# Performance work log

Measured on AMD Instinct MI355X. Metric: run time of the kernel, lower is better.

## Reference

```python
import jax, jax.numpy as jnp
import numpy as np

NUM_EMBEDDINGS = 4096
EMBEDDING_DIM = 128
COMMITMENT_COST = 0.25


def setup_inputs() -> dict:
    key = jax.random.key(0)
    k_x, k_w = jax.random.split(key)
    inputs = jax.random.normal(k_x, (32, 128, 32, 32), dtype=jnp.float32)
    # xavier_uniform for Embedding weight [K, D]: bound = sqrt(6/(K+D))
    bound = float(np.sqrt(6.0 / (NUM_EMBEDDINGS + EMBEDDING_DIM)))
    weight = jax.random.uniform(k_w, (NUM_EMBEDDINGS, EMBEDDING_DIM),
                                dtype=jnp.float32, minval=-bound, maxval=bound)
    return {"inputs": inputs, "weight": weight}


def reference(inputs, weight):
    K, D = weight.shape
    # channels-first 4D input with C == embedding_dim -> NHWC
    x = jnp.transpose(inputs, (0, 2, 3, 1))  # [B, H, W, D]
    input_shape = x.shape
    flat = x.reshape(-1, D)                  # [N, D]

    x_sq = jnp.sum(flat * flat, axis=1, keepdims=True)          # [N, 1]
    w_sq = jnp.sum(weight * weight, axis=1)                     # [K]
    two_xy = 2.0 * jnp.matmul(flat, weight.T)                   # [N, K]
    distances = x_sq - two_xy + w_sq[None, :] + 1e-8

    encoding_indices = jnp.argmin(distances, axis=1)            # [N] int

    quantized = weight[encoding_indices].reshape(input_shape)   # [B, H, W, D]

    q_latent_loss = jnp.mean((quantized - x) ** 2)
    e_latent_loss = jnp.mean((jax.lax.stop_gradient(quantized) - x) ** 2)
    loss = q_latent_loss + COMMITMENT_COST * e_latent_loss
    loss = jnp.where(jnp.isnan(loss) | jnp.isinf(loss), jnp.float32(0.1), loss)

    quantized_st = x + jax.lax.stop_gradient(quantized - x)

    counts = jnp.zeros((K,), dtype=jnp.float32).at[encoding_indices].add(1.0)
    avg_probs = counts / encoding_indices.shape[0]
    perplexity = jnp.exp(-jnp.sum(avg_probs * jnp.log(avg_probs + 1e-10)))

    encodings = jax.nn.one_hot(encoding_indices, K, dtype=jnp.float32)  # [N, K]

    # input was channels-first -> restore NCHW
    quantized_st = jnp.transpose(quantized_st, (0, 3, 1, 2))
    return quantized_st, loss, perplexity, encodings, encoding_indices
```

## Files before the change

### kernel.cpp

```cpp
#include <hip/hip_runtime.h>
#include <stdint.h>
#include <math.h>

#define K_CODES 4096
#define DIM 128
#define N_FLAT 32768
#define HW 1024

#define OFF_Q    0
#define OFF_LOSS 4194304
#define OFF_PERP 4194305
#define OFF_ENC  4194306
#define OFF_IDX  138412034

#define WS_PACKED 0
#define WS_COUNTS 262144
#define WS_WSQ    278528
#define WS_XSQ    294912
#define WS_PART   425984
#define WS_XHL    430080
#define WS_WHL    (WS_XHL + 16777216)

typedef _Float16 f16x8 __attribute__((ext_vector_type(8)));
typedef float    f32x4 __attribute__((ext_vector_type(4)));


__global__ __launch_bounds__(256) void wsq_kernel(const float* __restrict__ w,
                                                  float* __restrict__ wsq,
                                                  float* __restrict__ counts) {
    int wave = threadIdx.x >> 6, lane = threadIdx.x & 63;
    int k = blockIdx.x * 4 + wave;
    float a = w[k * DIM + lane];
    float b = w[k * DIM + lane + 64];
    float s = a * a + b * b;
    #pragma unroll
    for (int o = 32; o > 0; o >>= 1) s += __shfl_down(s, o, 64);
    if (lane == 0) { wsq[k] = s; counts[k] = 0.f; }
}

__global__ __launch_bounds__(256) void wplanes_kernel(const float* __restrict__ w,
                                                      _Float16* __restrict__ whl) {
    int T = blockIdx.x * 256 + threadIdx.x;
    int k = T >> 2, seg = T & 3;
    const float* wp = w + (size_t)k * DIM + seg * 32;
    _Float16* row = whl + (size_t)k * 256;
    #pragma unroll
    for (int q = 0; q < 4; ++q) {
        float4 a = *(const float4*)(wp + q * 8);
        float4 b = *(const float4*)(wp + q * 8 + 4);
        float vv[8] = {a.x, a.y, a.z, a.w, b.x, b.y, b.z, b.w};
        f16x8 hv, lv;
        #pragma unroll
        for (int j = 0; j < 8; ++j) {
            float v = 1024.0f * vv[j];
            _Float16 h = (_Float16)v;
            _Float16 l = (_Float16)(v - (float)h);
            hv[j] = h; lv[j] = l;
        }
        *(f16x8*)(row + seg * 32 + q * 8) = hv;
        *(f16x8*)(row + 128 + seg * 32 + q * 8) = lv;
    }
}

__global__ __launch_bounds__(256) void xprep_kernel(const float* __restrict__ x,
                                                    _Float16* __restrict__ xhl,
                                                    float* __restrict__ xsq,
                                                    unsigned long long* __restrict__ packed) {
    __shared__ float xt[128 * 65];
    const int t = threadIdx.x;
    const int n0 = blockIdx.x * 64;
    const int b = n0 >> 10, hw0 = n0 & 1023;
    const float* xg = x + (size_t)b * (DIM * HW) + hw0;
    #pragma unroll
    for (int i = 0; i < 16; ++i) {
        int idx = i * 256 + t;
        int c = idx >> 5, n2 = (idx & 31) << 1;
        float2 v = *(const float2*)(xg + c * HW + n2);
        xt[c * 65 + n2] = v.x;
        xt[c * 65 + n2 + 1] = v.y;
    }
    __syncthreads();
    if (t < 64) {
        packed[n0 + t] = ~0ull;
        float s = 0.f;
        #pragma unroll
        for (int c = 0; c < DIM; ++c) {
            float v = xt[c * 65 + t];
            s = fmaf(v, v, s);
        }
        xsq[n0 + t] = s;
    }
    const int n = t >> 2, seg = t & 3;
    _Float16* row = xhl + (size_t)(n0 + n) * 256;
    #pragma unroll
    for (int q = 0; q < 4; ++q) {
        f16x8 hv, lv;
        #pragma unroll
        for (int j = 0; j < 8; ++j) {
            float v = 32.0f * xt[(seg * 32 + q * 8 + j) * 65 + n];
            _Float16 h = (_Float16)v;
            _Float16 l = (_Float16)(v - (float)h);
            hv[j] = h; lv[j] = l;
        }
        *(f16x8*)(row + seg * 32 + q * 8) = hv;
        *(f16x8*)(row + 128 + seg * 32 + q * 8) = lv;
    }
}

__global__ __launch_bounds__(512) void dist_argmin(
    const _Float16* __restrict__ xhl, const _Float16* __restrict__ whl,
    const float* __restrict__ wsq, const float* __restrict__ xsq,
    unsigned long long* __restrict__ packed, float* __restrict__ enc)
{
    __shared__ __align__(16) char xlds[2][16384];
    __shared__ __align__(16) char wlds[2][16384];
    __shared__ float xsq_s[128];
    __shared__ unsigned long long red[128];

    const int tid  = threadIdx.x;
    const int lane = tid & 63, wave = tid >> 6;
    const int lq   = lane & 15, quad = lane >> 4;
    const int wn0  = (wave >> 2) * 64;
    const int wk0q = (wave & 3) * 32;
    const int n0   = blockIdx.x * 128;
    const int kbase = blockIdx.y * 512;

    const int r0 = wave * 16 + (lane >> 3);
    const int lc = (((lane & 7) ^ (lane >> 3)) << 4);
    const int lcAdj = lc + ((lc >> 6) * 192);
    const char* xB = (const char*)xhl;
    const char* wB = (const char*)whl;
    const size_t xrow0 = (size_t)(n0 + r0) * 512;

    const int swz  = (lq & 7) << 4;
    const int hoff = (quad << 4) ^ swz;
    const int loff = (64 | (quad << 4)) ^ swz;

    float* ebase = enc + (size_t)n0 * K_CODES + kbase;
    if (tid < 128) {
        float2 z2; z2.x = 0.f; z2.y = 0.f;
        *(float2*)(ebase + (size_t)tid * K_CODES) = z2;
        xsq_s[tid] = xsq[n0 + tid];
        red[tid] = ~0ull;
    }

#define GLOAD16(gp, lp) __builtin_amdgcn_global_load_lds(                      \
        (const __attribute__((address_space(1))) void*)(gp),                   \
        (__attribute__((address_space(3))) void*)(lp), 16, 0, 0)

    {
        const size_t wrow0 = (size_t)(kbase + r0) * 512;
        #pragma unroll
        for (int i = 0; i < 2; ++i) {
            GLOAD16(xB + xrow0 + (size_t)i * 4096 + lcAdj,
                    xlds[0] + wave * 2048 + i * 1024);
            GLOAD16(wB + wrow0 + (size_t)i * 4096 + lcAdj,
                    wlds[0] + wave * 2048 + i * 1024);
        }
    }

    f32x4 acc[4][2];
    float wk[2];

    for (int s = 0; s < 16; ++s) {
        const int p  = s & 1;
        const int ks = s >> 2, c0 = s & 3;
        const int k0 = kbase + ks * 128;
        if (c0 == 0) {
            wk[0] = wsq[k0 + wk0q + lq];
            wk[1] = wsq[k0 + wk0q + 16 + lq];
            #pragma unroll
            for (int i = 0; i < 4; ++i)
                #pragma unroll
                for (int j = 0; j < 2; ++j)
                    acc[i][j] = (f32x4){0.f, 0.f, 0.f, 0.f};
        }
        __syncthreads();

        f16x8 ah[4], al[4], bh[2], bl[2];
        const char* xb = xlds[p];
        const char* wb = wlds[p];
        #pragma unroll
        for (int i = 0; i < 4; ++i) {
            int xr = (wn0 + 16 * i + lq) * 128;
            ah[i] = *(const f16x8*)(xb + xr + hoff);
            al[i] = *(const f16x8*)(xb + xr + loff);
        }
        #pragma unroll
        for (int ki = 0; ki < 2; ++ki) {
            int wr = (wk0q + 16 * ki + lq) * 128;
            bh[ki] = *(const f16x8*)(wb + wr + hoff);
            bl[ki] = *(const f16x8*)(wb + wr + loff);
        }

        if (s < 15) {
            const int s1 = s + 1, ks1 = s1 >> 2, c01 = s1 & 3;
            const int offX = c01 * 64 + lcAdj;
            const size_t wrow0 = (size_t)(kbase + ks1 * 128 + r0) * 512;
            char* xd = xlds[p ^ 1] + wave * 2048;
            char* wd = wlds[p ^ 1] + wave * 2048;
            #pragma unroll
            for (int i = 0; i < 2; ++i) {
                GLOAD16(xB + xrow0 + (size_t)i * 4096 + offX, xd + i * 1024);
                GLOAD16(wB + wrow0 + (size_t)i * 4096 + offX, wd + i * 1024);
            }
        }

        {
            float4 z4; z4.x = z4.y = z4.z = z4.w = 0.f;
            #pragma unroll
            for (int j = 0; j < 2; ++j) {
                int idx = s * 1024 + j * 512 + tid;
                int r = idx >> 7, c4 = idx & 127;
                *(float4*)(ebase + (size_t)r * K_CODES + 2 + c4 * 4) = z4;
            }
        }

        #pragma unroll
        for (int ki = 0; ki < 2; ++ki)
            #pragma unroll
            for (int ni = 0; ni < 4; ++ni) {
                acc[ni][ki] = __builtin_amdgcn_mfma_f32_16x16x32_f16(
                    ah[ni], bh[ki], acc[ni][ki], 0, 0, 0);
                acc[ni][ki] = __builtin_amdgcn_mfma_f32_16x16x32_f16(
                    ah[ni], bl[ki], acc[ni][ki], 0, 0, 0);
                acc[ni][ki] = __builtin_amdgcn_mfma_f32_16x16x32_f16(
                    al[ni], bh[ki], acc[ni][ki], 0, 0, 0);
            }

        if (c0 == 3) {
            #pragma unroll
            for (int ni = 0; ni < 4; ++ni) {
                #pragma unroll
                for (int rg = 0; rg < 4; ++rg) {
                    int rowl = wn0 + ni * 16 + quad * 4 + rg;
                    float xr = xsq_s[rowl];
                    float best = 3.4e38f; int bk = 0;
                    #pragma unroll
                    for (int ki = 0; ki < 2; ++ki) {
                        int kl = wk0q + ki * 16 + lq;
                        float t = xr - acc[ni][ki][rg] * 6.103515625e-05f;
                        t += wk[ki];
                        t += 1e-8f;
                        if (t < best) { best = t; bk = k0 + kl; }
                    }
                    unsigned u = __float_as_uint(best);
                    u = (u & 0x80000000u) ? ~u : (u | 0x80000000u);
                    unsigned long long pck =
                        ((unsigned long long)u << 32) | (unsigned)bk;
                    #pragma unroll
                    for (int m = 1; m < 16; m <<= 1) {
                        unsigned long long o = __shfl_xor(pck, m, 64);
                        if (o < pck) pck = o;
                    }
                    if (lq == 0) atomicMin(&red[rowl], pck);
                }
            }
        }
    }
#undef GLOAD16

    __syncthreads();
    if (tid < 128) atomicMin(&packed[n0 + tid], red[tid]);
}

__global__ __launch_bounds__(256) void combine(
    const unsigned long long* __restrict__ packed,
    float* __restrict__ idxf, float* __restrict__ enc,
    float* __restrict__ counts)
{
    int n = blockIdx.x * 256 + threadIdx.x;
    unsigned k = (unsigned)(packed[n] & 0xFFFFFFFFu);
    idxf[n] = (float)k;
    enc[(size_t)n * K_CODES + k] = 1.0f;
    atomicAdd(&counts[k], 1.0f);
}

__global__ __launch_bounds__(256) void quantize_loss(
    const float* __restrict__ x, const float* __restrict__ w,
    const float* __restrict__ idxf, float* __restrict__ outq,
    float* __restrict__ part)
{
    const int base4 = (blockIdx.x * 256 + threadIdx.x) * 4;
    float s = 0.f;
    #pragma unroll
    for (int i = 0; i < 4; ++i) {
        int e  = base4 + i * 1048576;
        int hw = e & 1023;
        int c  = (e >> 10) & 127;
        int b  = e >> 17;
        int n  = (b << 10) | hw;
        float4 xv = *(const float4*)(x + e);
        float4 kf = *(const float4*)(idxf + n);
        float q0 = w[(int)kf.x * DIM + c];
        float q1 = w[(int)kf.y * DIM + c];
        float q2 = w[(int)kf.z * DIM + c];
        float q3 = w[(int)kf.w * DIM + c];
        float4 df; df.x = q0 - xv.x; df.y = q1 - xv.y;
                   df.z = q2 - xv.z; df.w = q3 - xv.w;
        float4 o;  o.x = xv.x + df.x; o.y = xv.y + df.y;
                   o.z = xv.z + df.z; o.w = xv.w + df.w;
        *(float4*)(outq + e) = o;
        s = fmaf(df.x, df.x, s);
        s = fmaf(df.y, df.y, s);
        s = fmaf(df.z, df.z, s);
        s = fmaf(df.w, df.w, s);
    }
    #pragma unroll
    for (int o = 32; o > 0; o >>= 1) s += __shfl_down(s, o, 64);
    __shared__ float ls[4];
    if ((threadIdx.x & 63) == 0) ls[threadIdx.x >> 6] = s;
    __syncthreads();
    if (threadIdx.x == 0) part[blockIdx.x] = ls[0] + ls[1] + ls[2] + ls[3];
}

__global__ __launch_bounds__(256) void finalize(
    const float* __restrict__ counts, const float* __restrict__ part,
    float* __restrict__ out)
{
    __shared__ float sh[512];
    float h = 0.f;
    for (int k = threadIdx.x; k < K_CODES; k += 256) {
        float p = counts[k] * (1.0f / N_FLAT);
        h += p * logf(p + 1e-10f);
    }
    float s = 0.f;
    for (int i = threadIdx.x; i < 1024; i += 256) s += part[i];
    sh[threadIdx.x] = h;
    sh[256 + threadIdx.x] = s;
    __syncthreads();
    #pragma unroll
    for (int st = 128; st > 0; st >>= 1) {
        if (threadIdx.x < st) {
            sh[threadIdx.x] += sh[threadIdx.x + st];
            sh[256 + threadIdx.x] += sh[256 + threadIdx.x + st];
        }
        __syncthreads();
    }
    if (threadIdx.x == 0) {
        float perp = expf(-sh[0]);
        float loss = 1.25f * (sh[256] / 4194304.0f);
        if (isnan(loss) || isinf(loss)) loss = 0.1f;
        out[OFF_LOSS] = loss;
        out[OFF_PERP] = perp;
    }
}

extern "C" void kernel_launch(void* const* d_in, const int* in_sizes, int n_in,
                              void* d_out, int out_size, void* d_ws, size_t ws_size,
                              hipStream_t stream) {
    const float* x = (const float*)d_in[0];
    const float* w = (const float*)d_in[1];
    float* out = (float*)d_out;
    char* ws = (char*)d_ws;

    unsigned long long* packed = (unsigned long long*)(ws + WS_PACKED);
    float* counts = (float*)(ws + WS_COUNTS);
    float* wsq    = (float*)(ws + WS_WSQ);
    float* xsq    = (float*)(ws + WS_XSQ);
    float* part   = (float*)(ws + WS_PART);
    _Float16* xhl = (_Float16*)(ws + WS_XHL);
    _Float16* whl = (_Float16*)(ws + WS_WHL);

    wsq_kernel<<<K_CODES / 4, 256, 0, stream>>>(w, wsq, counts);
    wplanes_kernel<<<K_CODES * 4 / 256, 256, 0, stream>>>(w, whl);
    xprep_kernel<<<N_FLAT / 64, 256, 0, stream>>>(x, xhl, xsq, packed);

    dim3 g2(256, 8);
    dist_argmin<<<g2, 512, 0, stream>>>(xhl, whl, wsq, xsq, packed,
                                        out + OFF_ENC);

    combine<<<N_FLAT / 256, 256, 0, stream>>>(packed, out + OFF_IDX,
                                              out + OFF_ENC, counts);

    quantize_loss<<<1024, 256, 0, stream>>>(x, w, out + OFF_IDX,
                                            out + OFF_Q, part);

    finalize<<<1, 256, 0, stream>>>(counts, part, out);
}
```

Measured before the change: 766.1 us.

## Widen code-range per block and remap grid for XCD-aware locality

Each block now covers 1024 codes instead of 512, halving the grid to 1024 blocks and doubling the K-loop to 32 stages. The 1D block index is remapped so consecutive x-tiles land on the same XCD, which should improve L2 reuse of the x data. The A-fragment LDS loads are moved inside the MFMA loop to cut register pressure. The encoding zero-fill is re-indexed to cover the wider code range. The risk is fewer blocks for load balance and extra LDS reads being exposed instead of hidden.

```diff
diff --git a/kernel.cpp b/kernel.cpp
--- a/kernel.cpp
+++ b/kernel.cpp
@@ -122,8 +122,13 @@
     const int lq   = lane & 15, quad = lane >> 4;
     const int wn0  = (wave >> 2) * 64;
     const int wk0q = (wave & 3) * 32;
-    const int n0   = blockIdx.x * 128;
-    const int kbase = blockIdx.y * 512;
+
+    const int id  = blockIdx.x;
+    const int xcd = id & 7, q = id >> 3;
+    const int y   = q & 3;
+    const int t   = (q >> 2) * 8 + xcd;
+    const int n0    = t * 128;
+    const int kbase = y * 1024;
 
     const int r0 = wave * 16 + (lane >> 3);
     const int lc = (((lane & 7) ^ (lane >> 3)) << 4);
@@ -162,7 +167,7 @@
     f32x4 acc[4][2];
     float wk[2];
 
-    for (int s = 0; s < 16; ++s) {
+    for (int s = 0; s < 32; ++s) {
         const int p  = s & 1;
         const int ks = s >> 2, c0 = s & 3;
         const int k0 = kbase + ks * 128;
@@ -177,15 +182,10 @@
         }
         __syncthreads();
 
-        f16x8 ah[4], al[4], bh[2], bl[2];
         const char* xb = xlds[p];
         const char* wb = wlds[p];
-        #pragma unroll
-        for (int i = 0; i < 4; ++i) {
-            int xr = (wn0 + 16 * i + lq) * 128;
-            ah[i] = *(const f16x8*)(xb + xr + hoff);
-            al[i] = *(const f16x8*)(xb + xr + loff);
-        }
+
+        f16x8 bh[2], bl[2];
         #pragma unroll
         for (int ki = 0; ki < 2; ++ki) {
             int wr = (wk0q + 16 * ki + lq) * 128;
@@ -193,7 +193,7 @@
             bl[ki] = *(const f16x8*)(wb + wr + loff);
         }
 
-        if (s < 15) {
+        if (s < 31) {
             const int s1 = s + 1, ks1 = s1 >> 2, c01 = s1 & 3;
             const int offX = c01 * 64 + lcAdj;
             const size_t wrow0 = (size_t)(kbase + ks1 * 128 + r0) * 512;
@@ -211,22 +211,26 @@
             #pragma unroll
             for (int j = 0; j < 2; ++j) {
                 int idx = s * 1024 + j * 512 + tid;
-                int r = idx >> 7, c4 = idx & 127;
+                int r = idx >> 8, c4 = idx & 255;
                 *(float4*)(ebase + (size_t)r * K_CODES + 2 + c4 * 4) = z4;
             }
         }
 
         #pragma unroll
-        for (int ki = 0; ki < 2; ++ki)
-            #pragma unroll
-            for (int ni = 0; ni < 4; ++ni) {
+        for (int ni = 0; ni < 4; ++ni) {
+            int xr = (wn0 + 16 * ni + lq) * 128;
+            f16x8 ah = *(const f16x8*)(xb + xr + hoff);
+            f16x8 al = *(const f16x8*)(xb + xr + loff);
+            #pragma unroll
+            for (int ki = 0; ki < 2; ++ki) {
                 acc[ni][ki] = __builtin_amdgcn_mfma_f32_16x16x32_f16(
-                    ah[ni], bh[ki], acc[ni][ki], 0, 0, 0);
+                    ah, bh[ki], acc[ni][ki], 0, 0, 0);
                 acc[ni][ki] = __builtin_amdgcn_mfma_f32_16x16x32_f16(
-                    ah[ni], bl[ki], acc[ni][ki], 0, 0, 0);
+                    ah, bl[ki], acc[ni][ki], 0, 0, 0);
                 acc[ni][ki] = __builtin_amdgcn_mfma_f32_16x16x32_f16(
-                    al[ni], bh[ki], acc[ni][ki], 0, 0, 0);
+                    al, bh[ki], acc[ni][ki], 0, 0, 0);
             }
+        }
 
         if (c0 == 3) {
             #pragma unroll
@@ -239,10 +243,10 @@
                     #pragma unroll
                     for (int ki = 0; ki < 2; ++ki) {
                         int kl = wk0q + ki * 16 + lq;
-                        float t = xr - acc[ni][ki][rg] * 6.103515625e-05f;
-                        t += wk[ki];
-                        t += 1e-8f;
-                        if (t < best) { best = t; bk = k0 + kl; }
+                        float tt = xr - acc[ni][ki][rg] * 6.103515625e-05f;
+                        tt += wk[ki];
+                        tt += 1e-8f;
+                        if (tt < best) { best = tt; bk = k0 + kl; }
                     }
                     unsigned u = __float_as_uint(best);
                     u = (u & 0x80000000u) ? ~u : (u | 0x80000000u);
@@ -366,9 +370,8 @@
     wplanes_kernel<<<K_CODES * 4 / 256, 256, 0, stream>>>(w, whl);
     xprep_kernel<<<N_FLAT / 64, 256, 0, stream>>>(x, xhl, xsq, packed);
 
-    dim3 g2(256, 8);
-    dist_argmin<<<g2, 512, 0, stream>>>(xhl, whl, wsq, xsq, packed,
-                                        out + OFF_ENC);
+    dist_argmin<<<1024, 512, 0, stream>>>(xhl, whl, wsq, xsq, packed,
+                                          out + OFF_ENC);
 
     combine<<<N_FLAT / 256, 256, 0, stream>>>(packed, out + OFF_IDX,
                                               out + OFF_ENC, counts);
```

New measurement: 758.8 us. No clear change (-1.0%).
